# Optimization experiments

Measured on AMD Instinct MI355X. Metric: run time of the kernel, lower is better.

Reference implementation:

```python
import jax, jax.numpy as jnp
from jax import lax
import numpy as np

NUM_HEADS = 12


def setup_inputs() -> dict:
    key = jax.random.key(0)
    ks = jax.random.split(key, 7)
    B, H, W, C = 8, 32, 32, 384
    x = jax.random.normal(ks[0], (B, H, W, C), dtype=jnp.float32)
    cls_token = jax.random.normal(ks[1], (B, 1, C), dtype=jnp.float32)
    qkv_w = jax.random.normal(ks[2], (3 * C, C), dtype=jnp.float32) * 0.02
    proj_w = jax.random.normal(ks[3], (C, C), dtype=jnp.float32) * 0.02
    proj_b = jax.random.normal(ks[4], (C,), dtype=jnp.float32) * 0.02
    lepe_w = jax.random.normal(ks[5], (C, 1, 5, 5), dtype=jnp.float32) * 0.02
    lepe_b = jax.random.normal(ks[6], (C,), dtype=jnp.float32) * 0.02
    return {"x": x, "cls_token": cls_token, "qkv_w": qkv_w,
            "proj_w": proj_w, "proj_b": proj_b,
            "lepe_w": lepe_w, "lepe_b": lepe_b}


def reference(x, cls_token, qkv_w, proj_w, proj_b, lepe_w, lepe_b):
    B, H, W, C = x.shape
    nh = NUM_HEADS
    hd = C // nh
    scale = hd ** (-0.5)

    x_seq = x.reshape(B, H * W, C)                      # [B, N, C]
    x_cat = jnp.concatenate([cls_token, x_seq], axis=1)  # [B, N+1, C]
    N1 = x_cat.shape[1]

    qkv = (x_cat @ qkv_w.T).reshape(B, N1, 3, nh, hd)
    qkv = qkv.transpose(2, 0, 3, 1, 4)                  # [3, B, h, N+1, d]
    q, k, v = qkv[0], qkv[1], qkv[2]

    attn = jnp.einsum('bhqd,bhkd->bhqk', q, k) * scale  # [B, h, N+1, N+1]
    attn = jax.nn.softmax(attn, axis=-1)
    out = jnp.einsum('bhqk,bhkd->bhqd', attn, v)        # [B, h, N+1, d]
    out = out.transpose(0, 2, 1, 3).reshape(B, N1, C)
    cls_out, x_out = out[:, :1, :], out[:, 1:, :]

    # LePE: 5x5 depthwise conv over the spatial grid (NCHW, groups=C)
    lepe = lax.conv_general_dilated(
        x.transpose(0, 3, 1, 2), lepe_w,
        window_strides=(1, 1), padding='SAME',
        feature_group_count=C,
        dimension_numbers=('NCHW', 'OIHW', 'NCHW'))
    lepe = lepe + lepe_b[None, :, None, None]
    lepe = lepe.transpose(0, 2, 3, 1).reshape(B, H * W, C)

    x_out = (x_out + lepe) @ proj_w.T + proj_b
    cls_out = cls_out @ proj_w.T + proj_b
    return x_out.reshape(B, H, W, C), cls_out
```

## Files before the change

kernel.cpp:

```cpp
#include <hip/hip_runtime.h>
#include <math.h>

#define NB 8
#define NHH 32
#define NWW 32
#define NC 384
#define NHEAD 12
#define NHD 32
#define NN1 1025
#define NHW 1024
#define NMROWS (NB * NN1)
#define MPAD 8320
#define NPB 1088
#define MP2 (NB * NPB)
#define NMT (MP2 / 64)
#define CST 1152

typedef float f32x4 __attribute__((ext_vector_type(4)));
typedef __bf16 bf16x8 __attribute__((ext_vector_type(8)));
typedef __attribute__((address_space(3))) unsigned int lds_u32;
typedef const __attribute__((address_space(1))) unsigned int glb_u32;

static __device__ __forceinline__ bf16x8 as_bf16x8(uint4 u) {
    union { uint4 a; bf16x8 b; } x; x.a = u; return x.b;
}
static __device__ __forceinline__ unsigned short bfbits(__bf16 b) {
    union { __bf16 a; unsigned short s; } u; u.a = b; return u.s;
}
static __device__ __forceinline__ float bf2f(unsigned short s) {
    union { unsigned u; float f; } x; x.u = ((unsigned)s) << 16; return x.f;
}
static __device__ __forceinline__ unsigned pack2(float a, float b) {
    return (unsigned)bfbits((__bf16)a) | ((unsigned)bfbits((__bf16)b) << 16);
}
static __device__ __forceinline__ int xcd_swz(int i, int nwg) {
    int xcd = i & 7, pos = i >> 3;
    int q = nwg >> 3, r = nwg & 7;
    return xcd * q + (xcd < r ? xcd : r) + pos;
}

#define P_N1 835584
#define P_N2 110592
#define P_N3 36864
#define P_N4 9600
#define P_N5 11520
#define P_TOT (P_N1 + P_N2 + P_N3 + P_N4 + P_N5)

__global__ __launch_bounds__(256) void prep_k(
    const float* __restrict__ x, const float* __restrict__ cls,
    const float* __restrict__ qkv_w, const float* __restrict__ proj_w,
    const float* __restrict__ lepe_w,
    __bf16* __restrict__ Ab, __bf16* __restrict__ wqb, __bf16* __restrict__ wpb,
    float* __restrict__ lepeT, __bf16* __restrict__ aob)
{
    int idx = blockIdx.x * 256 + threadIdx.x;
    if (idx >= P_TOT) return;
    if (idx < P_N1) {
        int e0 = idx * 4;
        int mp = e0 / NC, kk = e0 % NC;
        int b = mp / NPB, n = mp % NPB;
        float4 v = make_float4(0.f, 0.f, 0.f, 0.f);
        if (n < NN1) {
            const float* src = (n == 0) ? (cls + (size_t)b * NC + kk)
                                        : (x + ((size_t)(b * NHW + (n - 1))) * NC + kk);
            v = *(const float4*)src;
        }
        uint2 u; u.x = pack2(v.x, v.y); u.y = pack2(v.z, v.w);
        *(uint2*)(Ab + (size_t)mp * NC + kk) = u;
        return;
    }
    idx -= P_N1;
    if (idx < P_N2) {
        int e0 = idx * 4;
        float4 v = *(const float4*)(qkv_w + e0);
        uint2 u; u.x = pack2(v.x, v.y); u.y = pack2(v.z, v.w);
        *(uint2*)(wqb + e0) = u;
        return;
    }
    idx -= P_N2;
    if (idx < P_N3) {
        int e0 = idx * 4;
        float4 v = *(const float4*)(proj_w + e0);
        uint2 u; u.x = pack2(v.x, v.y); u.y = pack2(v.z, v.w);
        *(uint2*)(wpb + e0) = u;
        return;
    }
    idx -= P_N3;
    if (idx < P_N4) {
        int tap = idx / NC, cc = idx % NC;
        lepeT[tap * NC + cc] = lepe_w[cc * 25 + tap];
        return;
    }
    idx -= P_N4;
    {
        uint2 z; z.x = 0; z.y = 0;
        *(uint2*)(aob + (size_t)NMROWS * NC + idx * 4) = z;
    }
}

#define LP 72
#define QSCALE 0.25505654007f
#define CPD 136

union QkvSm {
    struct { __bf16 As[2][64][64]; __bf16 Bs[2][128][64]; } g;
    __bf16 C[64][CPD];
};

__global__ __launch_bounds__(256) void qkv_mfma_k(
    const __bf16* __restrict__ A, const __bf16* __restrict__ W,
    __bf16* __restrict__ Cg)
{
    __shared__ QkvSm sm;
    const int tid  = threadIdx.x;
    const int lane = tid & 63;
    const int wid  = tid >> 6;
    const int wr   = wid >> 1, wc = wid & 1;
    const int c    = lane & 15, hg = lane >> 4;
    const int wg   = xcd_swz(blockIdx.x, 9 * NMT);
    const int tile = wg % 9;
    const int m0   = (wg / 9) * 64;
    const int n0   = tile * 128;

    int aw_row[2], aw_col[2];
#pragma unroll
    for (int j = 0; j < 2; ++j) {
        int word = (wid * 2 + j) * 64 + lane;
        int row = word >> 3, slot = word & 7;
        aw_row[j] = row;
        aw_col[j] = (slot ^ (row & 7)) * 8;
    }
    int bw_row[4], bw_col[4];
#pragma unroll
    for (int j = 0; j < 4; ++j) {
        int word = (wid * 4 + j) * 64 + lane;
        int row = word >> 3, slot = word & 7;
        bw_row[j] = row;
        bw_col[j] = (slot ^ (row & 7)) * 8;
    }

    f32x4 acc[2][4];
#pragma unroll
    for (int i = 0; i < 2; ++i)
#pragma unroll
        for (int j = 0; j < 4; ++j) acc[i][j] = f32x4{0.f, 0.f, 0.f, 0.f};

    __bf16* asbase = &sm.g.As[0][0][0];
    __bf16* bsbase = &sm.g.Bs[0][0][0];

    auto stage = [&](int buf, int k0) {
#pragma unroll
        for (int j = 0; j < 2; ++j) {
            const __bf16* src = A + (size_t)(m0 + aw_row[j]) * NC + k0 + aw_col[j];
            __bf16* dst = asbase + (size_t)buf * 4096 + (wid * 2 + j) * 512;
            __builtin_amdgcn_global_load_lds((glb_u32*)src, (lds_u32*)dst, 16, 0, 0);
        }
#pragma unroll
        for (int j = 0; j < 4; ++j) {
            const __bf16* src = W + (size_t)(n0 + bw_row[j]) * NC + k0 + bw_col[j];
            __bf16* dst = bsbase + (size_t)buf * 8192 + (wid * 4 + j) * 512;
            __builtin_amdgcn_global_load_lds((glb_u32*)src, (lds_u32*)dst, 16, 0, 0);
        }
    };

    stage(0, 0);
    __syncthreads();

    for (int t = 0; t < 6; ++t) {
        const int cur = t & 1;
        if (t < 5) stage(cur ^ 1, (t + 1) * 64);

        const __bf16* ab = asbase + (size_t)cur * 4096;
        const __bf16* bb = bsbase + (size_t)cur * 8192;
#pragma unroll
        for (int ks = 0; ks < 2; ++ks) {
            bf16x8 af[2], bfr[4];
#pragma unroll
            for (int i = 0; i < 2; ++i) {
                int row = wr * 32 + i * 16 + c;
                int slot = (ks * 4 + hg) ^ (row & 7);
                af[i] = as_bf16x8(*(const uint4*)(ab + row * 64 + slot * 8));
            }
#pragma unroll
            for (int j = 0; j < 4; ++j) {
                int row = wc * 64 + j * 16 + c;
                int slot = (ks * 4 + hg) ^ (row & 7);
                bfr[j] = as_bf16x8(*(const uint4*)(bb + row * 64 + slot * 8));
            }
            __builtin_amdgcn_s_setprio(1);
#pragma unroll
            for (int i = 0; i < 2; ++i)
#pragma unroll
                for (int j = 0; j < 4; ++j)
                    acc[i][j] = __builtin_amdgcn_mfma_f32_16x16x32_bf16(
                        af[i], bfr[j], acc[i][j], 0, 0, 0);
            __builtin_amdgcn_s_setprio(0);
        }
        if (t < 5) __syncthreads();
    }

    __syncthreads();
    const float qs = (tile < 3) ? QSCALE : 1.0f;
#pragma unroll
    for (int i = 0; i < 2; ++i)
#pragma unroll
        for (int r = 0; r < 4; ++r) {
            int row = wr * 32 + i * 16 + 4 * hg + r;
#pragma unroll
            for (int j = 0; j < 4; ++j)
                sm.C[row][wc * 64 + j * 16 + c] = (__bf16)(acc[i][j][r] * qs);
        }
    __syncthreads();

#pragma unroll
    for (int it = 0; it < 4; ++it) {
        int idx   = it * 256 + tid;
        int row   = idx >> 4;
        int chunk = idx & 15;
        uint4 u = *(const uint4*)&sm.C[row][chunk * 8];
        *(uint4*)(Cg + (size_t)(m0 + row) * CST + n0 + chunk * 8) = u;
    }
}

__global__ __launch_bounds__(256) void proj_mfma_k(
    const __bf16* __restrict__ A, const __bf16* __restrict__ W,
    const float* __restrict__ bias, float* __restrict__ out)
{
    __shared__ __bf16 As[128][LP];
    __shared__ __bf16 Bs[64][LP];
    const int tid  = threadIdx.x;
    const int lane = tid & 63;
    const int wid  = tid >> 6;
    const int wr   = wid >> 1, wc = wid & 1;
    const int c    = lane & 15, hg = lane >> 4;
    const int wg   = xcd_swz(blockIdx.x, 6 * 65);
    const int m0   = (wg / 6) * 128;
    const int n0   = (wg % 6) * 64;
    const int srow = tid >> 1;
    const int scol = (tid & 1) * 32;
    const int brow = tid >> 2;
    const int bcol = (tid & 3) * 16;

    f32x4 acc[4][2];
#pragma unroll
    for (int i = 0; i < 4; ++i)
#pragma unroll
        for (int j = 0; j < 2; ++j) acc[i][j] = f32x4{0.f, 0.f, 0.f, 0.f};

    uint4 a4[4], b4[2];
#pragma unroll
    for (int s = 0; s < 4; ++s)
        a4[s] = *(const uint4*)(A + (size_t)(m0 + srow) * NC + scol + s * 8);
#pragma unroll
    for (int s = 0; s < 2; ++s)
        b4[s] = *(const uint4*)(W + (size_t)(n0 + brow) * NC + bcol + s * 8);

    for (int k0 = 0; k0 < NC; k0 += 64) {
        __syncthreads();
#pragma unroll
        for (int s = 0; s < 4; ++s) *(uint4*)&As[srow][scol + s * 8] = a4[s];
#pragma unroll
        for (int s = 0; s < 2; ++s) *(uint4*)&Bs[brow][bcol + s * 8] = b4[s];
        __syncthreads();
        if (k0 + 64 < NC) {
#pragma unroll
            for (int s = 0; s < 4; ++s)
                a4[s] = *(const uint4*)(A + (size_t)(m0 + srow) * NC + k0 + 64 + scol + s * 8);
#pragma unroll
            for (int s = 0; s < 2; ++s)
                b4[s] = *(const uint4*)(W + (size_t)(n0 + brow) * NC + k0 + 64 + bcol + s * 8);
        }
#pragma unroll
        for (int ks = 0; ks < 2; ++ks) {
            bf16x8 af[4], bfr[2];
#pragma unroll
            for (int i = 0; i < 4; ++i)
                af[i] = as_bf16x8(*(const uint4*)&As[wr * 64 + i * 16 + c][ks * 32 + hg * 8]);
#pragma unroll
            for (int j = 0; j < 2; ++j)
                bfr[j] = as_bf16x8(*(const uint4*)&Bs[wc * 32 + j * 16 + c][ks * 32 + hg * 8]);
#pragma unroll
            for (int i = 0; i < 4; ++i)
#pragma unroll
                for (int j = 0; j < 2; ++j)
                    acc[i][j] = __builtin_amdgcn_mfma_f32_16x16x32_bf16(
                        af[i], bfr[j], acc[i][j], 0, 0, 0);
        }
    }

#pragma unroll
    for (int i = 0; i < 4; ++i)
#pragma unroll
        for (int r = 0; r < 4; ++r) {
            int m = m0 + wr * 64 + i * 16 + 4 * hg + r;
            if (m >= NMROWS) continue;
            int b = m / NN1, n = m % NN1;
            float* dstrow = (n == 0)
                ? (out + (size_t)NB * NHW * NC + (size_t)b * NC)
                : (out + ((size_t)(b * NHW) + (n - 1)) * NC);
#pragma unroll
            for (int j = 0; j < 2; ++j) {
                int col = n0 + wc * 32 + j * 16 + c;
                dstrow[col] = acc[i][j][r] + bias[col];
            }
        }
}

#define KC 64
#define KPAD 40
#define VPAD 72
#define PPAD 72
#define NCH ((NN1 + KC - 1) / KC)

__global__ __launch_bounds__(256) void attn_mfma_k(
    const __bf16* __restrict__ Cg, __bf16* __restrict__ ao)
{
    __shared__ unsigned short Ks[2][KC][KPAD];
    __shared__ unsigned short Vs[2][32][VPAD];
    __shared__ unsigned short Ps[4][32][PPAD];

    const int wg    = xcd_swz(blockIdx.x, 9 * NB * NHEAD);
    const int qtile = wg % 9;
    const int bh    = wg / 9;
    const int b     = bh / NHEAD;
    const int hh    = bh % NHEAD;
    const int tid   = threadIdx.x;
    const int wv    = tid >> 6;
    const int lane  = tid & 63;
    const int c     = lane & 15;
    const int hg    = lane >> 4;
    const int q0    = qtile * 128 + wv * 32;
    const size_t MBp = (size_t)b * NPB;

    const __bf16* qb = Cg + hh * 32;
    const __bf16* kb = Cg + 384 + hh * 32;
    const __bf16* vb = Cg + 768 + hh * 32;

    uint4 zero4 = make_uint4(0, 0, 0, 0);
    bf16x8 qf[2];
#pragma unroll
    for (int qt = 0; qt < 2; ++qt) {
        int row = q0 + qt * 16 + c;
        uint4 u = (row < NN1)
            ? *(const uint4*)(qb + (MBp + row) * CST + hg * 8) : zero4;
        qf[qt] = as_bf16x8(u);
    }

    f32x4 O[2][2];
#pragma unroll
    for (int qt = 0; qt < 2; ++qt)
#pragma unroll
        for (int dt = 0; dt < 2; ++dt) O[qt][dt] = f32x4{0.f, 0.f, 0.f, 0.f};
    float lrun[2] = {0.f, 0.f};

    const int k_row = tid >> 2;
    const int k_col = (tid & 3) * 8;

    uint4 kr = *(const uint4*)(kb + (MBp + k_row) * CST + k_col);
    uint4 vr = *(const uint4*)(vb + (MBp + k_row) * CST + k_col);
    *(uint4*)&Ks[0][k_row][k_col] = kr;
    {
        union { uint4 u; unsigned short s[8]; } vu; vu.u = vr;
#pragma unroll
        for (int j = 0; j < 8; ++j) Vs[0][k_col + j][k_row] = vu.s[j];
    }
    __syncthreads();

    for (int t = 0; t < NCH; ++t) {
        const int kt0 = t * KC;
        const int cur = t & 1;
        const bool haveNext = (t + 1 < NCH);
        if (haveNext) {
            kr = *(const uint4*)(kb + (MBp + kt0 + KC + k_row) * CST + k_col);
            vr = *(const uint4*)(vb + (MBp + kt0 + KC + k_row) * CST + k_col);
        }
        const bool full = (kt0 + KC <= NN1);

        bf16x8 kf[4];
#pragma unroll
        for (int kt = 0; kt < 4; ++kt)
            kf[kt] = as_bf16x8(*(const uint4*)&Ks[cur][kt * 16 + c][hg * 8]);

#pragma unroll
        for (int qt = 0; qt < 2; ++qt) {
            f32x4 Sf[4];
            __builtin_amdgcn_s_setprio(1);
#pragma unroll
            for (int kt = 0; kt < 4; ++kt)
                Sf[kt] = __builtin_amdgcn_mfma_f32_16x16x32_bf16(
                    kf[kt], qf[qt], f32x4{0.f, 0.f, 0.f, 0.f}, 0, 0, 0);
            __builtin_amdgcn_s_setprio(0);

            if (!full) {
#pragma unroll
                for (int kt = 0; kt < 4; ++kt)
#pragma unroll
                    for (int r = 0; r < 4; ++r) {
                        int key = kt0 + kt * 16 + 4 * hg + r;
                        if (key >= NN1) Sf[kt][r] = -3.0e38f;
                    }
            }
            float psum = 0.f;
#pragma unroll
            for (int kt = 0; kt < 4; ++kt) {
                float p0 = exp2f(Sf[kt][0]);
                float p1 = exp2f(Sf[kt][1]);
                float p2 = exp2f(Sf[kt][2]);
                float p3 = exp2f(Sf[kt][3]);
                psum += (p0 + p1) + (p2 + p3);
                uint2 w; w.x = pack2(p0, p1); w.y = pack2(p2, p3);
                *(uint2*)&Ps[wv][qt * 16 + c][kt * 16 + 4 * hg] = w;
            }
            lrun[qt] += psum;
        }

        bf16x8 vf[2][2];
#pragma unroll
        for (int dt = 0; dt < 2; ++dt)
#pragma unroll
            for (int kh = 0; kh < 2; ++kh)
                vf[dt][kh] = as_bf16x8(*(const uint4*)&Vs[cur][dt * 16 + c][kh * 32 + hg * 8]);

        __builtin_amdgcn_s_setprio(1);
#pragma unroll
        for (int qt = 0; qt < 2; ++qt)
#pragma unroll
            for (int kh = 0; kh < 2; ++kh) {
                bf16x8 pa = as_bf16x8(*(const uint4*)&Ps[wv][qt * 16 + c][kh * 32 + hg * 8]);
#pragma unroll
                for (int dt = 0; dt < 2; ++dt)
                    O[qt][dt] = __builtin_amdgcn_mfma_f32_16x16x32_bf16(
                        pa, vf[dt][kh], O[qt][dt], 0, 0, 0);
            }
        __builtin_amdgcn_s_setprio(0);

        if (haveNext) {
            *(uint4*)&Ks[cur ^ 1][k_row][k_col] = kr;
            union { uint4 u; unsigned short s[8]; } vu; vu.u = vr;
#pragma unroll
            for (int j = 0; j < 8; ++j) Vs[cur ^ 1][k_col + j][k_row] = vu.s[j];
            __syncthreads();
        }
    }

#pragma unroll
    for (int qt = 0; qt < 2; ++qt) {
        float Ls = lrun[qt];
        Ls += __shfl_xor(Ls, 16);
        Ls += __shfl_xor(Ls, 32);
#pragma unroll
        for (int r = 0; r < 4; ++r) {
            float lr_ = __shfl(Ls, 4 * hg + r);
            int row = q0 + qt * 16 + 4 * hg + r;
            float inv = (lr_ > 0.f) ? 1.0f / lr_ : 0.f;
            if (row < NN1) {
#pragma unroll
                for (int dt = 0; dt < 2; ++dt)
                    ao[((size_t)(b * NN1 + row)) * NC + hh * NHD + dt * 16 + c]
                        = (__bf16)(O[qt][dt][r] * inv);
            }
        }
    }
}

__global__ __launch_bounds__(256) void lepe2_k(
    const float* __restrict__ x, const float* __restrict__ wT,
    const float* __restrict__ bias, __bf16* __restrict__ ao)
{
    int idx = blockIdx.x * 256 + threadIdx.x;
    if (idx >= NB * (NHH / 2) * NWW * (NC / 4)) return;
    int cg = idx % (NC / 4);
    int c4 = cg * 4;
    int pos = idx / (NC / 4);
    int ww = pos % NWW;
    int hp = (pos / NWW) % (NHH / 2);
    int b = pos / (NWW * (NHH / 2));
    int hh = hp * 2;

    float4 bv = *(const float4*)(bias + c4);
    float a0[2], a1[2], a2[2], a3[2];
    a0[0] = bv.x; a1[0] = bv.y; a2[0] = bv.z; a3[0] = bv.w;
    a0[1] = bv.x; a1[1] = bv.y; a2[1] = bv.z; a3[1] = bv.w;

#pragma unroll
    for (int i = 0; i < 6; ++i) {
        int y = hh + i - 2;
        bool yv = (unsigned)y < NHH;
#pragma unroll
        for (int j = 0; j < 5; ++j) {
            int xw = ww + j - 2;
            if (yv && (unsigned)xw < NWW) {
                float4 xv = *(const float4*)(x + (((size_t)b * NHH + y) * NWW + xw) * NC + c4);
                if (i < 5) {
                    float4 wv = *(const float4*)(wT + (i * 5 + j) * NC + c4);
                    a0[0] += xv.x * wv.x; a1[0] += xv.y * wv.y;
                    a2[0] += xv.z * wv.z; a3[0] += xv.w * wv.w;
                }
                if (i >= 1) {
                    float4 wv = *(const float4*)(wT + ((i - 1) * 5 + j) * NC + c4);
                    a0[1] += xv.x * wv.x; a1[1] += xv.y * wv.y;
                    a2[1] += xv.z * wv.z; a3[1] += xv.w * wv.w;
                }
            }
        }
    }

#pragma unroll
    for (int rr = 0; rr < 2; ++rr) {
        size_t m = (size_t)b * NN1 + 1 + (hh + rr) * NWW + ww;
        uint2* aop = (uint2*)(ao + m * NC + c4);
        uint2 old = *aop;
        float r0 = a0[rr] + bf2f((unsigned short)(old.x & 0xffff));
        float r1 = a1[rr] + bf2f((unsigned short)(old.x >> 16));
        float r2 = a2[rr] + bf2f((unsigned short)(old.y & 0xffff));
        float r3 = a3[rr] + bf2f((unsigned short)(old.y >> 16));
        uint2 nw; nw.x = pack2(r0, r1); nw.y = pack2(r2, r3);
        *aop = nw;
    }
}

extern "C" void kernel_launch(void* const* d_in, const int* in_sizes, int n_in,
                              void* d_out, int out_size, void* d_ws, size_t ws_size,
                              hipStream_t stream)
{
    const float* x      = (const float*)d_in[0];
    const float* cls    = (const float*)d_in[1];
    const float* qkv_w  = (const float*)d_in[2];
    const float* proj_w = (const float*)d_in[3];
    const float* proj_b = (const float*)d_in[4];
    const float* lepe_w = (const float*)d_in[5];
    const float* lepe_b = (const float*)d_in[6];
    float* out = (float*)d_out;
    char*  ws  = (char*)d_ws;

    size_t off = 0;
    __bf16* Ab    = (__bf16*)(ws + off); off += (size_t)MP2 * NC * 2;
    __bf16* wqb   = (__bf16*)(ws + off); off += (size_t)1152 * NC * 2;
    __bf16* wpb   = (__bf16*)(ws + off); off += (size_t)NC * NC * 2;
    float*  lepeT = (float*) (ws + off); off += (size_t)25 * NC * 4;
    __bf16* Cg    = (__bf16*)(ws + off); off += (size_t)MP2 * CST * 2;
    __bf16* aob   = (__bf16*)(ws + off); off += (size_t)MPAD * NC * 2;

    {
        prep_k<<<(P_TOT + 255) / 256, 256, 0, stream>>>(
            x, cls, qkv_w, proj_w, lepe_w, Ab, wqb, wpb, lepeT, aob);
    }
    {
        qkv_mfma_k<<<9 * NMT, 256, 0, stream>>>(Ab, wqb, Cg);
    }
    {
        attn_mfma_k<<<9 * NB * NHEAD, 256, 0, stream>>>(Cg, aob);
    }
    {
        int total = NB * (NHW / 2) * (NC / 4);
        lepe2_k<<<(total + 255) / 256, 256, 0, stream>>>(x, lepeT, lepe_b, aob);
    }
    {
        proj_mfma_k<<<6 * 65, 256, 0, stream>>>(aob, wpb, proj_b, out);
    }
}
```

Before: 125.6 us.

## Keep K fragments and softmax probabilities in registers instead of LDS

The attention kernel now loads K fragments straight from global memory into registers in MFMA layout, so the K shared-memory buffer is gone. The bf16 probabilities stay in registers and feed 16x16x16 MFMAs directly, which removes the P round-trip through LDS. The aim is to cut LDS traffic and LDS footprint, which may raise occupancy. In exchange each wave does its own redundant K global loads, register pressure rises, and the PV product uses twice as many smaller MFMA instructions.

```diff
diff --git a/kernel.cpp b/kernel.cpp
--- a/kernel.cpp
+++ b/kernel.cpp
@@ -18,6 +18,8 @@
 
 typedef float f32x4 __attribute__((ext_vector_type(4)));
 typedef __bf16 bf16x8 __attribute__((ext_vector_type(8)));
+typedef __bf16 bf16x4 __attribute__((ext_vector_type(4)));
+typedef short s16x4 __attribute__((ext_vector_type(4)));
 typedef __attribute__((address_space(3))) unsigned int lds_u32;
 typedef const __attribute__((address_space(1))) unsigned int glb_u32;
 
@@ -32,6 +34,14 @@
 }
 static __device__ __forceinline__ unsigned pack2(float a, float b) {
     return (unsigned)bfbits((__bf16)a) | ((unsigned)bfbits((__bf16)b) << 16);
+}
+static __device__ __forceinline__ f32x4 mfma16(bf16x4 a, bf16x4 b, f32x4 c) {
+#if __has_builtin(__builtin_amdgcn_mfma_f32_16x16x16_bf16)
+    return __builtin_amdgcn_mfma_f32_16x16x16_bf16(a, b, c, 0, 0, 0);
+#else
+    union { bf16x4 h; s16x4 s; } ua, ub; ua.h = a; ub.h = b;
+    return __builtin_amdgcn_mfma_f32_16x16x16bf16_1k(ua.s, ub.s, c, 0, 0, 0);
+#endif
 }
 static __device__ __forceinline__ int xcd_swz(int i, int nwg) {
     int xcd = i & 7, pos = i >> 3;
@@ -307,17 +317,13 @@
 }
 
 #define KC 64
-#define KPAD 40
 #define VPAD 72
-#define PPAD 72
 #define NCH ((NN1 + KC - 1) / KC)
 
 __global__ __launch_bounds__(256) void attn_mfma_k(
     const __bf16* __restrict__ Cg, __bf16* __restrict__ ao)
 {
-    __shared__ unsigned short Ks[2][KC][KPAD];
     __shared__ unsigned short Vs[2][32][VPAD];
-    __shared__ unsigned short Ps[4][32][PPAD];
 
     const int wg    = xcd_swz(blockIdx.x, 9 * NB * NHEAD);
     const int qtile = wg % 9;
@@ -325,8 +331,8 @@
     const int b     = bh / NHEAD;
     const int hh    = bh % NHEAD;
     const int tid   = threadIdx.x;
+    const int lane  = tid & 63;
     const int wv    = tid >> 6;
-    const int lane  = tid & 63;
     const int c     = lane & 15;
     const int hg    = lane >> 4;
     const int q0    = qtile * 128 + wv * 32;
@@ -356,9 +362,11 @@
     const int k_row = tid >> 2;
     const int k_col = (tid & 3) * 8;
 
-    uint4 kr = *(const uint4*)(kb + (MBp + k_row) * CST + k_col);
+    uint4 kcur[4], knxt[4];
+#pragma unroll
+    for (int kt = 0; kt < 4; ++kt)
+        kcur[kt] = *(const uint4*)(kb + (MBp + kt * 16 + c) * CST + hg * 8);
     uint4 vr = *(const uint4*)(vb + (MBp + k_row) * CST + k_col);
-    *(uint4*)&Ks[0][k_row][k_col] = kr;
     {
         union { uint4 u; unsigned short s[8]; } vu; vu.u = vr;
 #pragma unroll
@@ -371,16 +379,14 @@
         const int cur = t & 1;
         const bool haveNext = (t + 1 < NCH);
         if (haveNext) {
-            kr = *(const uint4*)(kb + (MBp + kt0 + KC + k_row) * CST + k_col);
+#pragma unroll
+            for (int kt = 0; kt < 4; ++kt)
+                knxt[kt] = *(const uint4*)(kb + (MBp + kt0 + KC + kt * 16 + c) * CST + hg * 8);
             vr = *(const uint4*)(vb + (MBp + kt0 + KC + k_row) * CST + k_col);
         }
         const bool full = (kt0 + KC <= NN1);
 
-        bf16x8 kf[4];
-#pragma unroll
-        for (int kt = 0; kt < 4; ++kt)
-            kf[kt] = as_bf16x8(*(const uint4*)&Ks[cur][kt * 16 + c][hg * 8]);
-
+        bf16x4 pa[2][4];
 #pragma unroll
         for (int qt = 0; qt < 2; ++qt) {
             f32x4 Sf[4];
@@ -388,7 +394,7 @@
 #pragma unroll
             for (int kt = 0; kt < 4; ++kt)
                 Sf[kt] = __builtin_amdgcn_mfma_f32_16x16x32_bf16(
-                    kf[kt], qf[qt], f32x4{0.f, 0.f, 0.f, 0.f}, 0, 0, 0);
+                    as_bf16x8(kcur[kt]), qf[qt], f32x4{0.f, 0.f, 0.f, 0.f}, 0, 0, 0);
             __builtin_amdgcn_s_setprio(0);
 
             if (!full) {
@@ -408,37 +414,34 @@
                 float p2 = exp2f(Sf[kt][2]);
                 float p3 = exp2f(Sf[kt][3]);
                 psum += (p0 + p1) + (p2 + p3);
-                uint2 w; w.x = pack2(p0, p1); w.y = pack2(p2, p3);
-                *(uint2*)&Ps[wv][qt * 16 + c][kt * 16 + 4 * hg] = w;
+                pa[qt][kt] = bf16x4{(__bf16)p0, (__bf16)p1, (__bf16)p2, (__bf16)p3};
             }
             lrun[qt] += psum;
         }
 
-        bf16x8 vf[2][2];
+        bf16x4 vbf[2][4];
 #pragma unroll
         for (int dt = 0; dt < 2; ++dt)
 #pragma unroll
-            for (int kh = 0; kh < 2; ++kh)
-                vf[dt][kh] = as_bf16x8(*(const uint4*)&Vs[cur][dt * 16 + c][kh * 32 + hg * 8]);
+            for (int kt = 0; kt < 4; ++kt)
+                vbf[dt][kt] = *(const bf16x4*)&Vs[cur][dt * 16 + c][kt * 16 + 4 * hg];
 
         __builtin_amdgcn_s_setprio(1);
 #pragma unroll
         for (int qt = 0; qt < 2; ++qt)
 #pragma unroll
-            for (int kh = 0; kh < 2; ++kh) {
-                bf16x8 pa = as_bf16x8(*(const uint4*)&Ps[wv][qt * 16 + c][kh * 32 + hg * 8]);
-#pragma unroll
-                for (int dt = 0; dt < 2; ++dt)
-                    O[qt][dt] = __builtin_amdgcn_mfma_f32_16x16x32_bf16(
-                        pa, vf[dt][kh], O[qt][dt], 0, 0, 0);
-            }
+            for (int dt = 0; dt < 2; ++dt)
+#pragma unroll
+                for (int kt = 0; kt < 4; ++kt)
+                    O[qt][dt] = mfma16(pa[qt][kt], vbf[dt][kt], O[qt][dt]);
         __builtin_amdgcn_s_setprio(0);
 
         if (haveNext) {
-            *(uint4*)&Ks[cur ^ 1][k_row][k_col] = kr;
             union { uint4 u; unsigned short s[8]; } vu; vu.u = vr;
 #pragma unroll
             for (int j = 0; j < 8; ++j) Vs[cur ^ 1][k_col + j][k_row] = vu.s[j];
+#pragma unroll
+            for (int kt = 0; kt < 4; ++kt) kcur[kt] = knxt[kt];
             __syncthreads();
         }
     }
```

After: 127.2 us. About the same (+1.3%).
